# Performance work log

Measured on AMD Instinct MI355X. Metric: run time of the kernel, lower is better.

The kernel has to match this reference:

```python
import jax, jax.numpy as jnp
import numpy as np

LATENT_DIM = 512
NUM_EMBEDDINGS = 4096
COMMITMENT_COST = 0.25
N_TOKENS = 32768


def setup_inputs() -> dict:
    key = jax.random.key(0)
    k_z, k_e = jax.random.split(key)
    z = jax.random.normal(k_z, (N_TOKENS, LATENT_DIM), dtype=jnp.float32)
    # embedding.weight ~ U(-1/K, 1/K), matching the torch init
    emb = jax.random.uniform(
        k_e, (NUM_EMBEDDINGS, LATENT_DIM), dtype=jnp.float32,
        minval=-1.0 / NUM_EMBEDDINGS, maxval=1.0 / NUM_EMBEDDINGS)
    return {"z": z, "emb": emb}


def reference(z, emb):
    flat_z = z.reshape(-1, LATENT_DIM)  # [N, D]
    # squared L2 distances: ||z||^2 + ||e||^2 - 2 z.e^T  -> [N, K]
    distances = (
        jnp.sum(flat_z ** 2, axis=1, keepdims=True)
        + jnp.sum(emb ** 2, axis=1)
        - 2.0 * jnp.matmul(flat_z, emb.T)
    )
    encoding_indices = jnp.argmin(distances, axis=1)  # [N]
    quantized = emb[encoding_indices].reshape(z.shape)  # [N, D]

    q_latent_loss = jnp.mean((jax.lax.stop_gradient(quantized) - z) ** 2)
    commitment_loss = jnp.mean((quantized - jax.lax.stop_gradient(z)) ** 2)
    vq_loss = q_latent_loss + COMMITMENT_COST * commitment_loss

    # codebook usage perplexity (histogram instead of dense one-hot)
    n = flat_z.shape[0]
    counts = jnp.zeros((NUM_EMBEDDINGS,), jnp.float32).at[encoding_indices].add(1.0)
    avg_probs = counts / n
    perplexity = jnp.exp(-jnp.sum(avg_probs * jnp.log(avg_probs + 1e-10)))

    # straight-through estimator
    quantized_st = z + jax.lax.stop_gradient(quantized - z)
    return quantized_st, vq_loss, perplexity
```

## Files before the change

kernel.cpp:

```cpp
#include <hip/hip_runtime.h>

#define NTOK   32768
#define DIM    512
#define NCODE  4096
#define NELEM  (NTOK*DIM)
#define COMMIT 0.25
#define ESCALE 8192.0f
#define EINV   (1.0f/4096.0f)
#define KSCL   262144.0f
#define KOFF   65536.0f

#define OFF_Z8      0ULL
#define OFF_E8      16777216ULL
#define OFF_EN32    18874368ULL
#define OFF_ROWMIN  18890752ULL
#define OFF_COUNTS  19021824ULL
#define OFF_SSE     19038208ULL

typedef int   v8i  __attribute__((ext_vector_type(8)));
typedef float v16f __attribute__((ext_vector_type(16)));

#define GLOBAL_AS __attribute__((address_space(1)))
#define LDS_AS    __attribute__((address_space(3)))

__device__ __forceinline__ void gld16(const void* g, void* l) {
    __builtin_amdgcn_global_load_lds((const GLOBAL_AS unsigned int*)g,
                                     (LDS_AS unsigned int*)l, 16, 0, 0);
}

__global__ void conv_kernel(const float* __restrict__ z, const float* __restrict__ e,
                            unsigned* __restrict__ z8, unsigned* __restrict__ e8,
                            unsigned* __restrict__ counts, double* __restrict__ sse) {
    const int ZI = NELEM / 16;
    const int TI = ZI + (NCODE * DIM) / 16;
    int i = blockIdx.x * blockDim.x + threadIdx.x;
    if (i < NCODE) counts[i] = 0u;
    if (i < 256)   sse[i] = 0.0;
    if (i >= TI) return;
    const float4* src; unsigned* dst; int j; float sc;
    if (i < ZI) { src = (const float4*)z; dst = z8; j = i; sc = 1.0f; }
    else        { src = (const float4*)e; dst = e8; j = i - ZI; sc = ESCALE; }
    uint4 o;
#pragma unroll
    for (int q = 0; q < 4; q++) {
        float4 v = src[j * 4 + q];
        int r = 0;
        r = __builtin_amdgcn_cvt_pk_fp8_f32(v.x * sc, v.y * sc, r, false);
        r = __builtin_amdgcn_cvt_pk_fp8_f32(v.z * sc, v.w * sc, r, true);
        (&o.x)[q] = (unsigned)r;
    }
    ((uint4*)dst)[j] = o;
}

__global__ void enorm_kernel(const float* __restrict__ emb, float* __restrict__ en32) {
    int gw = (blockIdx.x * blockDim.x + threadIdx.x) >> 6;
    int lane = threadIdx.x & 63;
    if (gw >= NCODE) return;
    const float4* p = (const float4*)(emb + (size_t)gw * DIM);
    float4 a = p[lane * 2], b = p[lane * 2 + 1];
    double s = (double)a.x*a.x + (double)a.y*a.y + (double)a.z*a.z + (double)a.w*a.w
             + (double)b.x*b.x + (double)b.y*b.y + (double)b.z*b.z + (double)b.w*b.w;
    for (int off = 32; off; off >>= 1) s += __shfl_down(s, off);
    if (lane == 0) en32[gw] = (float)s;
}

__global__ __launch_bounds__(256)
void score_pass(const unsigned char* __restrict__ z8, const unsigned char* __restrict__ e8,
                const float* __restrict__ en32,
                unsigned* __restrict__ rowmin) {
    __shared__ __align__(16) unsigned char sZ[64 * 512];
    __shared__ __align__(16) unsigned char sE[64 * 512];
    const int tid = threadIdx.x;
    const int row0 = blockIdx.x * 64;
    const int wv = tid >> 6, ln = tid & 63;
    const int wm = wv & 1;
    const int wn = wv >> 1;
    const int c = ln & 31, h = ln >> 5;

#pragma unroll
    for (int s = 0; s < 8; s++) {
        int q = wv * 8 + s;
        int r = 2 * q + h;
        unsigned g = (unsigned)((ln & 31) ^ (r & 31));
        gld16(z8 + (size_t)(row0 + r) * 512 + g * 16u, sZ + q * 1024);
    }

    unsigned eoff[8];
    unsigned char* lE[8];
#pragma unroll
    for (int s = 0; s < 8; s++) {
        int q = wv * 8 + s;
        int r = 2 * q + h;
        unsigned g = (unsigned)((ln & 31) ^ (r & 31));
        eoff[s] = (unsigned)(r * 512) + g * 16u;
        lE[s] = sE + q * 1024;
    }

    v16f acc0, acc1;
    unsigned runmin[16];
#pragma unroll
    for (int reg = 0; reg < 16; reg++) runmin[reg] = 0xFFFFFFFFu;

    const int mrow = (wm * 32 + c) * 512;
    const int nrow = (wn * 32 + c) * 512;

    for (int ct = 0; ct < 64; ct++) {
        __syncthreads();
        const unsigned char* ebase = e8 + (size_t)ct * (64 * 512);
#pragma unroll
        for (int s = 0; s < 8; s++) gld16(ebase + eoff[s], lE[s]);
        float en = en32[ct * 64 + wn * 32 + c];
        __syncthreads();

        acc0 = (v16f)(0.0f); acc1 = (v16f)(0.0f);
#pragma unroll
        for (int kt = 0; kt < 8; kt++) {
            int G = kt * 4 + 2 * h;
            uint4 x0 = *(const uint4*)(sZ + mrow + (((G    ) ^ c) * 16));
            uint4 x1 = *(const uint4*)(sZ + mrow + (((G + 1) ^ c) * 16));
            v8i a = (v8i){(int)x0.x, (int)x0.y, (int)x0.z, (int)x0.w,
                          (int)x1.x, (int)x1.y, (int)x1.z, (int)x1.w};
            uint4 y0 = *(const uint4*)(sE + nrow + (((G    ) ^ c) * 16));
            uint4 y1 = *(const uint4*)(sE + nrow + (((G + 1) ^ c) * 16));
            v8i b = (v8i){(int)y0.x, (int)y0.y, (int)y0.z, (int)y0.w,
                          (int)y1.x, (int)y1.y, (int)y1.z, (int)y1.w};
            if (kt & 1)
                acc1 = __builtin_amdgcn_mfma_scale_f32_32x32x64_f8f6f4(
                    a, b, acc1, 0, 0, 0, 0x7F, 0, 0x7F);
            else
                acc0 = __builtin_amdgcn_mfma_scale_f32_32x32x64_f8f6f4(
                    a, b, acc0, 0, 0, 0, 0x7F, 0, 0x7F);
        }

        unsigned n = (unsigned)(ct * 64 + wn * 32 + c);
#pragma unroll
        for (int reg = 0; reg < 16; reg++) {
            float s = en - (acc0[reg] + acc1[reg]) * EINV;
            unsigned kq = (unsigned)fmaf(s, KSCL, KOFF);
            unsigned p = (kq << 12) | n;
            runmin[reg] = runmin[reg] < p ? runmin[reg] : p;
        }
    }

    __syncthreads();
    unsigned* tmp = (unsigned*)sZ;
#pragma unroll
    for (int reg = 0; reg < 16; reg++) {
        unsigned v = runmin[reg];
#pragma unroll
        for (int off = 1; off < 32; off <<= 1) {
            unsigned o = (unsigned)__shfl_xor((int)v, off);
            v = v < o ? v : o;
        }
        if (c == 0) {
            int rr = (reg & 3) + 8 * (reg >> 2) + 4 * h;
            tmp[(wm * 2 + wn) * 32 + rr] = v;
        }
    }
    __syncthreads();
    if (tid < 64) {
        int wmb = tid >> 5, rr = tid & 31;
        unsigned v0 = tmp[(wmb * 2 + 0) * 32 + rr];
        unsigned v1 = tmp[(wmb * 2 + 1) * 32 + rr];
        rowmin[row0 + tid] = v0 < v1 ? v0 : v1;
    }
}

__global__ void gather_loss(const float* __restrict__ z, const float* __restrict__ emb,
                            const unsigned* __restrict__ rowmin,
                            float* __restrict__ out, double* __restrict__ sse,
                            unsigned* __restrict__ counts) {
    int i = blockIdx.x * blockDim.x + threadIdx.x;
    float4 zv = ((const float4*)z)[i];
    int row = i >> 7, col = i & 127;
    unsigned code = rowmin[row] & 0xFFFu;
    if (col == 0) atomicAdd(&counts[code], 1u);
    float4 q = ((const float4*)emb)[code * 128 + col];
    float4 dv = make_float4(q.x - zv.x, q.y - zv.y, q.z - zv.z, q.w - zv.w);
    float4 o  = make_float4(zv.x + dv.x, zv.y + dv.y, zv.z + dv.z, zv.w + dv.w);
    ((float4*)out)[i] = o;
    double loc = (double)dv.x*dv.x + (double)dv.y*dv.y + (double)dv.z*dv.z + (double)dv.w*dv.w;
    for (int off = 32; off; off >>= 1) loc += __shfl_down(loc, off);
    __shared__ double sw[4];
    if ((threadIdx.x & 63) == 0) sw[threadIdx.x >> 6] = loc;
    __syncthreads();
    if (threadIdx.x == 0)
        atomicAdd(&sse[blockIdx.x & 255], sw[0] + sw[1] + sw[2] + sw[3]);
}

__global__ void finalize(const unsigned* __restrict__ counts, const double* __restrict__ sse,
                         float* __restrict__ out) {
    __shared__ double sh[256], sv[256];
    double h = 0.0;
    for (int b = threadIdx.x; b < NCODE; b += 256) {
        double p = (double)counts[b] / (double)NTOK;
        h += p * log(p + 1e-10);
    }
    sh[threadIdx.x] = h;
    sv[threadIdx.x] = sse[threadIdx.x];
    __syncthreads();
    for (int off = 128; off > 0; off >>= 1) {
        if (threadIdx.x < off) {
            sh[threadIdx.x] += sh[threadIdx.x + off];
            sv[threadIdx.x] += sv[threadIdx.x + off];
        }
        __syncthreads();
    }
    if (threadIdx.x == 0) {
        out[NELEM]     = (float)((1.0 + COMMIT) * sv[0] / (double)NELEM);
        out[NELEM + 1] = (float)exp(-sh[0]);
    }
}

extern "C" void kernel_launch(void* const* d_in, const int* in_sizes, int n_in,
                              void* d_out, int out_size, void* d_ws, size_t ws_size,
                              hipStream_t stream) {
    const float* z   = (const float*)d_in[0];
    const float* emb = (const float*)d_in[1];
    float* out = (float*)d_out;
    char* ws = (char*)d_ws;

    unsigned* z8 = (unsigned*)(ws + OFF_Z8);
    unsigned* e8 = (unsigned*)(ws + OFF_E8);
    float*    en32 = (float*)(ws + OFF_EN32);
    unsigned* rowmin = (unsigned*)(ws + OFF_ROWMIN);
    unsigned* counts = (unsigned*)(ws + OFF_COUNTS);
    double*   sse    = (double*)(ws + OFF_SSE);

    conv_kernel<<<(NELEM/16 + (NCODE*DIM)/16 + 255) / 256, 256, 0, stream>>>(
        z, emb, z8, e8, counts, sse);
    enorm_kernel<<<(NCODE * 64) / 256, 256, 0, stream>>>(emb, en32);

    score_pass<<<NTOK / 64, 256, 0, stream>>>((const unsigned char*)z8,
                                              (const unsigned char*)e8, en32, rowmin);

    gather_loss<<<NELEM / 4 / 256, 256, 0, stream>>>(z, emb, rowmin, out, sse, counts);
    finalize<<<1, 256, 0, stream>>>(counts, sse, out);
}
```

Baseline: 247.2 us.

## Double-buffer codebook tiles in score pass and keep z fragments in registers

Keeps the z tile's MFMA operands in registers after a single LDS read, freeing its LDS buffer. That buffer and a second one then act as ping-pong buffers for codebook tiles, with asynchronous global-to-LDS loads for tile ct+2 issued while tile ct is computed. Codebook norms are also staged into LDS once per block. The aim is to hide global load latency and remove the two full barriers per tile, at the cost of more registers and about 80KB of LDS per block under a launch bound requesting 2 blocks per CU.

```diff
diff --git a/kernel.cpp b/kernel.cpp
--- a/kernel.cpp
+++ b/kernel.cpp
@@ -64,12 +64,13 @@
     if (lane == 0) en32[gw] = (float)s;
 }
 
-__global__ __launch_bounds__(256)
+__global__ __launch_bounds__(256, 2)
 void score_pass(const unsigned char* __restrict__ z8, const unsigned char* __restrict__ e8,
                 const float* __restrict__ en32,
                 unsigned* __restrict__ rowmin) {
-    __shared__ __align__(16) unsigned char sZ[64 * 512];
-    __shared__ __align__(16) unsigned char sE[64 * 512];
+    __shared__ __align__(16) unsigned char sB0[64 * 512];
+    __shared__ __align__(16) unsigned char sB1[64 * 512];
+    __shared__ __align__(16) float sEn[NCODE];
     const int tid = threadIdx.x;
     const int row0 = blockIdx.x * 64;
     const int wv = tid >> 6, ln = tid & 63;
@@ -82,54 +83,76 @@
         int q = wv * 8 + s;
         int r = 2 * q + h;
         unsigned g = (unsigned)((ln & 31) ^ (r & 31));
-        gld16(z8 + (size_t)(row0 + r) * 512 + g * 16u, sZ + q * 1024);
+        gld16(z8 + (size_t)(row0 + r) * 512 + g * 16u, sB1 + q * 1024);
+    }
+#pragma unroll
+    for (int s = 0; s < 4; s++) {
+        int chunk = wv * 4 + s;
+        gld16((const unsigned char*)en32 + chunk * 1024 + (unsigned)(ln * 16),
+              (unsigned char*)sEn + chunk * 1024);
     }
 
     unsigned eoff[8];
-    unsigned char* lE[8];
 #pragma unroll
     for (int s = 0; s < 8; s++) {
         int q = wv * 8 + s;
         int r = 2 * q + h;
         unsigned g = (unsigned)((ln & 31) ^ (r & 31));
         eoff[s] = (unsigned)(r * 512) + g * 16u;
-        lE[s] = sE + q * 1024;
-    }
-
-    v16f acc0, acc1;
-    unsigned runmin[16];
-#pragma unroll
-    for (int reg = 0; reg < 16; reg++) runmin[reg] = 0xFFFFFFFFu;
+    }
+
+    __builtin_amdgcn_sched_barrier(0);
+
+#pragma unroll
+    for (int s = 0; s < 8; s++)
+        gld16(e8 + eoff[s], sB0 + (wv * 8 + s) * 1024);
+
+    asm volatile("s_waitcnt vmcnt(8)" ::: "memory");
+    __builtin_amdgcn_s_barrier();
 
     const int mrow = (wm * 32 + c) * 512;
     const int nrow = (wn * 32 + c) * 512;
+    v8i za[8];
+#pragma unroll
+    for (int kt = 0; kt < 8; kt++) {
+        int G = kt * 4 + 2 * h;
+        uint4 x0 = *(const uint4*)(sB1 + mrow + (((G    ) ^ c) * 16));
+        uint4 x1 = *(const uint4*)(sB1 + mrow + (((G + 1) ^ c) * 16));
+        za[kt] = (v8i){(int)x0.x, (int)x0.y, (int)x0.z, (int)x0.w,
+                       (int)x1.x, (int)x1.y, (int)x1.z, (int)x1.w};
+    }
+    asm volatile("s_waitcnt lgkmcnt(0)" ::: "memory");
+    __builtin_amdgcn_s_barrier();
+
+#pragma unroll
+    for (int s = 0; s < 8; s++)
+        gld16(e8 + 32768 + eoff[s], sB1 + (wv * 8 + s) * 1024);
+
+    unsigned runmin[16];
+#pragma unroll
+    for (int reg = 0; reg < 16; reg++) runmin[reg] = 0xFFFFFFFFu;
 
     for (int ct = 0; ct < 64; ct++) {
-        __syncthreads();
-        const unsigned char* ebase = e8 + (size_t)ct * (64 * 512);
-#pragma unroll
-        for (int s = 0; s < 8; s++) gld16(ebase + eoff[s], lE[s]);
-        float en = en32[ct * 64 + wn * 32 + c];
-        __syncthreads();
-
-        acc0 = (v16f)(0.0f); acc1 = (v16f)(0.0f);
+        if (ct == 63) asm volatile("s_waitcnt vmcnt(0)" ::: "memory");
+        else          asm volatile("s_waitcnt vmcnt(8)" ::: "memory");
+        __builtin_amdgcn_s_barrier();
+
+        const unsigned char* sB = (ct & 1) ? sB1 : sB0;
+        float en = sEn[ct * 64 + wn * 32 + c];
+        v16f acc0 = (v16f)(0.0f), acc1 = (v16f)(0.0f);
 #pragma unroll
         for (int kt = 0; kt < 8; kt++) {
             int G = kt * 4 + 2 * h;
-            uint4 x0 = *(const uint4*)(sZ + mrow + (((G    ) ^ c) * 16));
-            uint4 x1 = *(const uint4*)(sZ + mrow + (((G + 1) ^ c) * 16));
-            v8i a = (v8i){(int)x0.x, (int)x0.y, (int)x0.z, (int)x0.w,
-                          (int)x1.x, (int)x1.y, (int)x1.z, (int)x1.w};
-            uint4 y0 = *(const uint4*)(sE + nrow + (((G    ) ^ c) * 16));
-            uint4 y1 = *(const uint4*)(sE + nrow + (((G + 1) ^ c) * 16));
+            uint4 y0 = *(const uint4*)(sB + nrow + (((G    ) ^ c) * 16));
+            uint4 y1 = *(const uint4*)(sB + nrow + (((G + 1) ^ c) * 16));
             v8i b = (v8i){(int)y0.x, (int)y0.y, (int)y0.z, (int)y0.w,
                           (int)y1.x, (int)y1.y, (int)y1.z, (int)y1.w};
             if (kt & 1)
                 acc1 = __builtin_amdgcn_mfma_scale_f32_32x32x64_f8f6f4(
-                    a, b, acc1, 0, 0, 0, 0x7F, 0, 0x7F);
+                    za[kt], b, acc1, 0, 0, 0, 0x7F, 0, 0x7F);
             else
                 acc0 = __builtin_amdgcn_mfma_scale_f32_32x32x64_f8f6f4(
-                    a, b, acc0, 0, 0, 0, 0x7F, 0, 0x7F);
+                    za[kt], b, acc0, 0, 0, 0, 0x7F, 0, 0x7F);
         }
 
         unsigned n = (unsigned)(ct * 64 + wn * 32 + c);
@@ -140,10 +163,21 @@
             unsigned p = (kq << 12) | n;
             runmin[reg] = runmin[reg] < p ? runmin[reg] : p;
         }
-    }
-
-    __syncthreads();
-    unsigned* tmp = (unsigned*)sZ;
+
+        asm volatile("s_waitcnt lgkmcnt(0)" ::: "memory");
+        __builtin_amdgcn_s_barrier();
+
+        if (ct < 62) {
+            unsigned char* sD = (ct & 1) ? sB1 : sB0;
+            const unsigned char* ebase = e8 + (size_t)(ct + 2) * 32768;
+#pragma unroll
+            for (int s = 0; s < 8; s++)
+                gld16(ebase + eoff[s], sD + (wv * 8 + s) * 1024);
+        }
+    }
+
+    __syncthreads();
+    unsigned* tmp = (unsigned*)sB0;
 #pragma unroll
     for (int reg = 0; reg < 16; reg++) {
         unsigned v = runmin[reg];
```

Measured after the change: 227.8 us. 7.8% less time.
